# Optimization experiments

Hardware: AMD Instinct MI355X
Metric: run time of the kernel (lower is better)

## Reference

```python
import jax, jax.numpy as jnp
import numpy as np

V, D, H, LYR, W, L, B = 32000, 1024, 16, 4, 256, 2048, 1
HD = D // H          # 64
I = 3280             # _round_to_multiple(3.2*D, 8)
EPS = 1e-5
STD = 0.01
CLAMP = 50.0


def rmsnorm(x, w):
    # RMSNorm with clamp/eps/isfinite guards as in the torch module
    x = jnp.clip(x.astype(jnp.float32), -10000.0, 10000.0)
    rms = jnp.sqrt(jnp.maximum(jnp.mean(x * x, axis=-1, keepdims=True), EPS) + EPS)
    out = x / rms * w
    return jnp.where(jnp.isfinite(out), out, 0.0)


def attention(x, wq_w, wq_b, wk_w, wk_b, wv_w, wv_b, wo_w, wo_b, qn_w, kn_w):
    Bx, Lx, Dx = x.shape
    def proj(w, b):
        return (x @ w.T + b).reshape(Bx, Lx, H, HD).transpose(0, 2, 1, 3)  # (B,H,L,hd)
    q = rmsnorm(proj(wq_w, wq_b), qn_w)
    k = rmsnorm(proj(wk_w, wk_b), kn_w)
    v = proj(wv_w, wv_b)
    i = jnp.arange(Lx)
    # causal + sliding-window: mask out j > i  OR  i - j >= window
    invalid = (i[None, :] > i[:, None]) | ((i[:, None] - i[None, :]) >= W)
    scores = jnp.einsum('bhqd,bhkd->bhqk', q, k) * (HD ** -0.5)
    scores = jnp.where(invalid[None, None], -jnp.inf, scores)
    probs = jax.nn.softmax(scores, axis=-1)
    out = jnp.einsum('bhqk,bhkd->bhqd', probs, v)
    out = jnp.where(jnp.isfinite(out), out, 0.0)
    out = out.transpose(0, 2, 1, 3).reshape(Bx, Lx, Dx)
    return out @ wo_w.T + wo_b


def swiglu(x, w1_w, w1_b, w2_w, w2_b, w3_w, w3_b):
    z1 = x @ w1_w.T + w1_b
    z3 = x @ w3_w.T + w3_b
    return (jax.nn.silu(z1) * z3) @ w2_w.T + w2_b


def setup_inputs() -> dict:
    key = jax.random.key(0)
    ks = jax.random.split(key, 12)
    nrm = lambda k, s: jax.random.normal(k, s, jnp.float32) * STD
    return {
        'tokens': jax.random.randint(ks[0], (B, L), 0, V, dtype=jnp.int32),
        'embed_w': nrm(ks[1], (V, D)),
        'ln1_w': jnp.ones((LYR, D), jnp.float32),
        'ln2_w': jnp.ones((LYR, D), jnp.float32),
        'wq_w': nrm(ks[2], (LYR, D, D)), 'wq_b': jnp.zeros((LYR, D), jnp.float32),
        'wk_w': nrm(ks[3], (LYR, D, D)), 'wk_b': jnp.zeros((LYR, D), jnp.float32),
        'wv_w': nrm(ks[4], (LYR, D, D)), 'wv_b': jnp.zeros((LYR, D), jnp.float32),
        'wo_w': nrm(ks[5], (LYR, D, D)), 'wo_b': jnp.zeros((LYR, D), jnp.float32),
        'qn_w': jnp.ones((LYR, HD), jnp.float32),
        'kn_w': jnp.ones((LYR, HD), jnp.float32),
        'w1_w': nrm(ks[6], (LYR, I, D)), 'w1_b': jnp.zeros((LYR, I), jnp.float32),
        'w2_w': nrm(ks[7], (LYR, D, I)), 'w2_b': jnp.zeros((LYR, D), jnp.float32),
        'w3_w': nrm(ks[8], (LYR, I, D)), 'w3_b': jnp.zeros((LYR, I), jnp.float32),
        'lnf_w': jnp.ones((D,), jnp.float32),
        'lm_w': nrm(ks[9], (V, D)), 'lm_b': jnp.zeros((V,), jnp.float32),
    }


def reference(tokens, embed_w, ln1_w, ln2_w, wq_w, wq_b, wk_w, wk_b, wv_w, wv_b,
              wo_w, wo_b, qn_w, kn_w, w1_w, w1_b, w2_w, w2_b, w3_w, w3_b,
              lnf_w, lm_w, lm_b):
    x = embed_w[tokens]  # (B,L,D)
    for l in range(LYR):
        x = x + attention(rmsnorm(x, ln1_w[l]),
                          wq_w[l], wq_b[l], wk_w[l], wk_b[l], wv_w[l], wv_b[l],
                          wo_w[l], wo_b[l], qn_w[l], kn_w[l])
        x = x + swiglu(rmsnorm(x, ln2_w[l]),
                       w1_w[l], w1_b[l], w2_w[l], w2_b[l], w3_w[l], w3_b[l])
    x = rmsnorm(x, lnf_w)
    logits = x @ lm_w.T + lm_b
    return jnp.clip(logits, -CLAMP, CLAMP)
```

## Files before the change

### kernel.cpp

```cpp
#include <hip/hip_runtime.h>
#include <hip/hip_bf16.h>
#include <math.h>

#define Dm   1024
#define Hn   16
#define HDm  64
#define Lm   2048
#define Wm   256
#define Im   3280
#define Vm   32000
#define NLAYER 4
#define EPSf 1e-5f

typedef unsigned short ushort;
typedef __attribute__((ext_vector_type(8))) short bf16x8;
typedef __attribute__((ext_vector_type(4))) float f32x4;

static __device__ __forceinline__ float clamp10k(float x) {
    return fminf(fmaxf(x, -10000.0f), 10000.0f);
}

static __device__ __forceinline__ ushort f2bf(float f) {
    __hip_bfloat16 h = __float2bfloat16(f);
    return *reinterpret_cast<ushort*>(&h);
}

static __device__ __forceinline__ void gload16(const ushort* g, ushort* l) {
    __builtin_amdgcn_global_load_lds(
        (const __attribute__((address_space(1))) void*)(const void*)g,
        (__attribute__((address_space(3))) void*)(void*)l, 16, 0, 0);
}

__global__ __launch_bounds__(256) void embed_k(const int* __restrict__ tok,
                                               const float* __restrict__ ew,
                                               float* __restrict__ x) {
    int i = blockIdx.x;
    int t = tok[i];
    const float4* src = (const float4*)(ew + (size_t)t * Dm);
    float4* dst = (float4*)(x + (size_t)i * Dm);
    dst[threadIdx.x] = src[threadIdx.x];
}

__global__ __launch_bounds__(256) void rmsnorm_row(const float* __restrict__ x,
                                                   const float* __restrict__ w,
                                                   ushort* __restrict__ out) {
    __shared__ float red[256];
    int row = blockIdx.x, tid = threadIdx.x;
    float4 vx = ((const float4*)(x + (size_t)row * Dm))[tid];
    vx.x = clamp10k(vx.x); vx.y = clamp10k(vx.y);
    vx.z = clamp10k(vx.z); vx.w = clamp10k(vx.w);
    float ss = vx.x * vx.x + vx.y * vx.y + vx.z * vx.z + vx.w * vx.w;
    red[tid] = ss;
    __syncthreads();
    for (int s = 128; s > 0; s >>= 1) {
        if (tid < s) red[tid] += red[tid + s];
        __syncthreads();
    }
    float mean = red[0] * (1.0f / Dm);
    float inv = 1.0f / sqrtf(fmaxf(mean, EPSf) + EPSf);
    float4 vw = ((const float4*)w)[tid];
    float o0 = vx.x * inv * vw.x;
    float o1 = vx.y * inv * vw.y;
    float o2 = vx.z * inv * vw.z;
    float o3 = vx.w * inv * vw.w;
    if (!isfinite(o0)) o0 = 0.0f;
    if (!isfinite(o1)) o1 = 0.0f;
    if (!isfinite(o2)) o2 = 0.0f;
    if (!isfinite(o3)) o3 = 0.0f;
    ushort4 o;
    o.x = f2bf(o0); o.y = f2bf(o1); o.z = f2bf(o2); o.w = f2bf(o3);
    ((ushort4*)(out + (size_t)row * Dm))[tid] = o;
}

__global__ __launch_bounds__(256) void rmsnorm_head_bf16(const float* __restrict__ qk,
                                                         const float* __restrict__ w,
                                                         ushort* __restrict__ out) {
    int wave = threadIdx.x >> 6, lane = threadIdx.x & 63;
    int r = blockIdx.x * 4 + wave;
    int i = r >> 4, h = r & 15;
    float xv = clamp10k(qk[(size_t)r * HDm + lane]);
    float ss = xv * xv;
#pragma unroll
    for (int off = 32; off >= 1; off >>= 1) ss += __shfl_xor(ss, off, 64);
    float mean = ss * (1.0f / HDm);
    float inv = 1.0f / sqrtf(fmaxf(mean, EPSf) + EPSf);
    float o = xv * inv * w[lane];
    if (!isfinite(o)) o = 0.0f;
    out[((size_t)h * Lm + i) * HDm + lane] = f2bf(o);
}

__global__ __launch_bounds__(256) void vtrans_k(const float* __restrict__ vb,
                                                ushort* __restrict__ vt) {
    __shared__ ushort tile[64 * 72];
    int i0 = blockIdx.x * 64, h = blockIdx.y;
    int t = threadIdx.x;
    int r = t >> 2, q4 = t & 3;
    const float4* src = (const float4*)(vb + (size_t)(i0 + r) * Dm + h * HDm);
#pragma unroll
    for (int k = 0; k < 4; ++k) {
        int c4 = q4 + k * 4;
        float4 v = src[c4];
        int c = c4 * 4;
        tile[(c + 0) * 72 + r] = f2bf(v.x);
        tile[(c + 1) * 72 + r] = f2bf(v.y);
        tile[(c + 2) * 72 + r] = f2bf(v.z);
        tile[(c + 3) * 72 + r] = f2bf(v.w);
    }
    __syncthreads();
    int d = t >> 2, ch = t & 3;
    uint4 a = *(const uint4*)&tile[d * 72 + ch * 16];
    uint4 b = *(const uint4*)&tile[d * 72 + ch * 16 + 8];
    ushort* dst = vt + ((size_t)(h * HDm + d)) * Lm + i0 + ch * 16;
    *(uint4*)dst = a;
    *(uint4*)(dst + 8) = b;
}

__global__ __launch_bounds__(256) void attn_mfma(const ushort* __restrict__ qh,
                                                 const ushort* __restrict__ kh,
                                                 const ushort* __restrict__ vt,
                                                 ushort* __restrict__ out) {
    __shared__ ushort Ks[32 * 72];
    __shared__ ushort Vs[64 * 40];
    __shared__ ushort Pl[4][16 * 40];

    const int tid  = threadIdx.x;
    const int wave = tid >> 6;
    const int lane = tid & 63;
    const int l15  = lane & 15;
    const int quad = lane >> 4;
    const int h    = blockIdx.y;
    const int q0   = blockIdx.x * 64;
    const int qw   = q0 + wave * 16;
    const int qmy  = qw + l15;

    const ushort* qbase = qh + ((size_t)h * Lm + qw + l15) * HDm;
    bf16x8 qf0 = *(const bf16x8*)(qbase + quad * 8);
    bf16x8 qf1 = *(const bf16x8*)(qbase + 32 + quad * 8);

    f32x4 o0 = {0.f, 0.f, 0.f, 0.f}, o1 = o0, o2 = o0, o3 = o0;
    float m = -1e4f, lsum = 0.0f;

    const int krow = tid >> 3, kch = tid & 7;
    const int vrow = tid >> 2, vch = tid & 3;
    const ushort* kg = kh + ((size_t)h * Lm + krow) * HDm + kch * 8;
    const ushort* vg = vt + ((size_t)(h * HDm + vrow)) * Lm + vch * 8;

    int tlo = q0 - 256; if (tlo < 0) tlo = 0;

    for (int t0 = tlo; t0 < q0 + 64; t0 += 32) {
        __syncthreads();
        *(uint4*)&Ks[krow * 72 + kch * 8] = *(const uint4*)(kg + (size_t)t0 * HDm);
        *(uint4*)&Vs[vrow * 40 + vch * 8] = *(const uint4*)(vg + t0);
        __syncthreads();

        if (t0 <= qw + 15 && t0 + 31 >= qw - 255) {
            bf16x8 k00 = *(const bf16x8*)&Ks[l15 * 72 + quad * 8];
            bf16x8 k01 = *(const bf16x8*)&Ks[l15 * 72 + 32 + quad * 8];
            bf16x8 k10 = *(const bf16x8*)&Ks[(l15 + 16) * 72 + quad * 8];
            bf16x8 k11 = *(const bf16x8*)&Ks[(l15 + 16) * 72 + 32 + quad * 8];
            f32x4 s0 = {0.f, 0.f, 0.f, 0.f}, s1 = s0;
            s0 = __builtin_amdgcn_mfma_f32_16x16x32_bf16(k00, qf0, s0, 0, 0, 0);
            s0 = __builtin_amdgcn_mfma_f32_16x16x32_bf16(k01, qf1, s0, 0, 0, 0);
            s1 = __builtin_amdgcn_mfma_f32_16x16x32_bf16(k10, qf0, s1, 0, 0, 0);
            s1 = __builtin_amdgcn_mfma_f32_16x16x32_bf16(k11, qf1, s1, 0, 0, 0);

            float sv[8];
            bool full = (t0 + 31 <= qw) && (t0 >= qw - 240);
            int jb = t0 + quad * 4;
            if (full) {
#pragma unroll
                for (int r = 0; r < 4; ++r) {
                    sv[r]     = s0[r] * 0.125f;
                    sv[r + 4] = s1[r] * 0.125f;
                }
            } else {
#pragma unroll
                for (int r = 0; r < 4; ++r) {
                    int ja = jb + r, jc = jb + 16 + r;
                    sv[r]     = (ja <= qmy && ja >= qmy - 255) ? s0[r] * 0.125f : -1e30f;
                    sv[r + 4] = (jc <= qmy && jc >= qmy - 255) ? s1[r] * 0.125f : -1e30f;
                }
            }

            float rm = sv[0];
#pragma unroll
            for (int r = 1; r < 8; ++r) rm = fmaxf(rm, sv[r]);
            rm = fmaxf(rm, __shfl_xor(rm, 16));
            rm = fmaxf(rm, __shfl_xor(rm, 32));
            float mn = fmaxf(m, rm);
            float alpha = __expf(m - mn);
            float p[8], ps = 0.f;
#pragma unroll
            for (int r = 0; r < 8; ++r) { p[r] = __expf(sv[r] - mn); ps += p[r]; }
            ps += __shfl_xor(ps, 16);
            ps += __shfl_xor(ps, 32);
            lsum = lsum * alpha + ps;
            m = mn;

            ushort4 pk0, pk1;
            pk0.x = f2bf(p[0]); pk0.y = f2bf(p[1]); pk0.z = f2bf(p[2]); pk0.w = f2bf(p[3]);
            pk1.x = f2bf(p[4]); pk1.y = f2bf(p[5]); pk1.z = f2bf(p[6]); pk1.w = f2bf(p[7]);
            *(ushort4*)&Pl[wave][l15 * 40 + quad * 4]      = pk0;
            *(ushort4*)&Pl[wave][l15 * 40 + 16 + quad * 4] = pk1;
            asm volatile("s_waitcnt lgkmcnt(0)" ::: "memory");
            bf16x8 pa  = *(const bf16x8*)&Pl[wave][l15 * 40 + quad * 8];
            bf16x8 vf0 = *(const bf16x8*)&Vs[l15 * 40 + quad * 8];
            bf16x8 vf1 = *(const bf16x8*)&Vs[(l15 + 16) * 40 + quad * 8];
            bf16x8 vf2 = *(const bf16x8*)&Vs[(l15 + 32) * 40 + quad * 8];
            bf16x8 vf3 = *(const bf16x8*)&Vs[(l15 + 48) * 40 + quad * 8];

            float a0 = __shfl(alpha, quad * 4 + 0);
            float a1 = __shfl(alpha, quad * 4 + 1);
            float a2 = __shfl(alpha, quad * 4 + 2);
            float a3 = __shfl(alpha, quad * 4 + 3);
            o0[0] *= a0; o0[1] *= a1; o0[2] *= a2; o0[3] *= a3;
            o1[0] *= a0; o1[1] *= a1; o1[2] *= a2; o1[3] *= a3;
            o2[0] *= a0; o2[1] *= a1; o2[2] *= a2; o2[3] *= a3;
            o3[0] *= a0; o3[1] *= a1; o3[2] *= a2; o3[3] *= a3;

            o0 = __builtin_amdgcn_mfma_f32_16x16x32_bf16(pa, vf0, o0, 0, 0, 0);
            o1 = __builtin_amdgcn_mfma_f32_16x16x32_bf16(pa, vf1, o1, 0, 0, 0);
            o2 = __builtin_amdgcn_mfma_f32_16x16x32_bf16(pa, vf2, o2, 0, 0, 0);
            o3 = __builtin_amdgcn_mfma_f32_16x16x32_bf16(pa, vf3, o3, 0, 0, 0);
        }
    }

    float linv = 1.0f / lsum;
    ushort* ob = out + (size_t)(qw + quad * 4) * Dm + h * HDm + l15;
#pragma unroll
    for (int r = 0; r < 4; ++r) {
        float li = __shfl(linv, quad * 4 + r);
        size_t off = (size_t)r * Dm;
        ob[off]      = f2bf(o0[r] * li);
        ob[off + 16] = f2bf(o1[r] * li);
        ob[off + 32] = f2bf(o2[r] * li);
        ob[off + 48] = f2bf(o3[r] * li);
    }
}

__global__ __launch_bounds__(256) void convert_w(const float* __restrict__ src,
                                                 ushort* __restrict__ dst,
                                                 int N, int K, int Kp) {
    int n = blockIdx.y;
    int k = blockIdx.x * 256 + threadIdx.x;
    if (k >= Kp) return;
    float v = 0.0f;
    if (n < N && k < K) v = src[(size_t)n * K + k];
    dst[(size_t)n * Kp + k] = f2bf(v);
}

__global__ __launch_bounds__(256) void gemm_bf16(const ushort* __restrict__ A,
                                                 const ushort* __restrict__ Wb,
                                                 const float* __restrict__ bias,
                                                 float* __restrict__ C,
                                                 int K, int N, int ldc, int act) {
    __shared__ ushort As[128 * 32];
    __shared__ ushort Bs[128 * 32];
    const int tid = threadIdx.x;
    const int wave = tid >> 6;
    const int lane = tid & 63;
    const int lane15 = lane & 15;
    const int quad = lane >> 4;
    const int rowBlk = blockIdx.y * 128;
    const int colBlk = blockIdx.x * 128;
    const int wm = (wave >> 1) * 64;
    const int wn = (wave & 1) * 64;

    const int srow = lane >> 2;
    const int scol = (lane & 3) * 8;

    const ushort* aSrc0 = A + (size_t)(rowBlk + wave * 32 + srow) * K + scol;
    const ushort* bSrc0 = Wb + (size_t)(colBlk + wave * 32 + srow) * K + scol;
    ushort* aDst0 = &As[(wave * 32) * 32];
    ushort* aDst1 = &As[(wave * 32 + 16) * 32];
    ushort* bDst0 = &Bs[(wave * 32) * 32];
    ushort* bDst1 = &Bs[(wave * 32 + 16) * 32];

    f32x4 acc[4][4];
#pragma unroll
    for (int i = 0; i < 4; ++i)
#pragma unroll
        for (int j = 0; j < 4; ++j) acc[i][j] = (f32x4){0.f, 0.f, 0.f, 0.f};

    for (int k0 = 0; k0 < K; k0 += 32) {
        __syncthreads();
        gload16(aSrc0 + k0, aDst0);
        gload16(aSrc0 + k0 + (size_t)16 * K, aDst1);
        gload16(bSrc0 + k0, bDst0);
        gload16(bSrc0 + k0 + (size_t)16 * K, bDst1);
        __syncthreads();

        bf16x8 a[4], b[4];
#pragma unroll
        for (int im = 0; im < 4; ++im)
            a[im] = *(const bf16x8*)&As[(wm + im * 16 + lane15) * 32 + quad * 8];
#pragma unroll
        for (int in = 0; in < 4; ++in)
            b[in] = *(const bf16x8*)&Bs[(wn + in * 16 + lane15) * 32 + quad * 8];
#pragma unroll
        for (int im = 0; im < 4; ++im)
#pragma unroll
            for (int in = 0; in < 4; ++in)
                acc[im][in] = __builtin_amdgcn_mfma_f32_16x16x32_bf16(
                    a[im], b[in], acc[im][in], 0, 0, 0);
    }

#pragma unroll
    for (int im = 0; im < 4; ++im) {
        int r0 = rowBlk + wm + im * 16 + quad * 4;
#pragma unroll
        for (int in = 0; in < 4; ++in) {
            int c = colBlk + wn + in * 16 + lane15;
            if (c < N) {
                float bia = bias[c];
#pragma unroll
                for (int reg = 0; reg < 4; ++reg) {
                    float v = acc[im][in][reg] + bia;
                    if (act) v = fminf(fmaxf(v, -50.0f), 50.0f);
                    C[(size_t)(r0 + reg) * ldc + c] = v;
                }
            }
        }
    }
}

__global__ __launch_bounds__(256) void add_k(float* __restrict__ x,
                                             const float* __restrict__ t, int n4) {
    int i = blockIdx.x * 256 + threadIdx.x;
    if (i < n4) {
        float4 a = ((const float4*)x)[i];
        float4 b = ((const float4*)t)[i];
        a.x += b.x; a.y += b.y; a.z += b.z; a.w += b.w;
        ((float4*)x)[i] = a;
    }
}

__global__ __launch_bounds__(256) void swiglu_k(const float* __restrict__ z1,
                                                const float* __restrict__ z3,
                                                ushort* __restrict__ z1b) {
    int row = blockIdx.x, tid = threadIdx.x;
    const float* a = z1 + (size_t)row * Im;
    const float* b = z3 + (size_t)row * Im;
    ushort* o = z1b + (size_t)row * 3296;
    for (int c = tid; c < 3296; c += 256) {
        float v = 0.0f;
        if (c < Im) {
            float x = a[c];
            v = x / (1.0f + expf(-x)) * b[c];
        }
        o[c] = f2bf(v);
    }
}

extern "C" void kernel_launch(void* const* d_in, const int* in_sizes, int n_in,
                              void* d_out, int out_size, void* d_ws, size_t ws_size,
                              hipStream_t stream) {
    const int*   tokens  = (const int*)  d_in[0];
    const float* embed_w = (const float*)d_in[1];
    const float* ln1_w   = (const float*)d_in[2];
    const float* ln2_w   = (const float*)d_in[3];
    const float* wq_w    = (const float*)d_in[4];
    const float* wq_b    = (const float*)d_in[5];
    const float* wk_w    = (const float*)d_in[6];
    const float* wk_b    = (const float*)d_in[7];
    const float* wv_w    = (const float*)d_in[8];
    const float* wv_b    = (const float*)d_in[9];
    const float* wo_w    = (const float*)d_in[10];
    const float* wo_b    = (const float*)d_in[11];
    const float* qn_w    = (const float*)d_in[12];
    const float* kn_w    = (const float*)d_in[13];
    const float* w1_w    = (const float*)d_in[14];
    const float* w1_b    = (const float*)d_in[15];
    const float* w2_w    = (const float*)d_in[16];
    const float* w2_b    = (const float*)d_in[17];
    const float* w3_w    = (const float*)d_in[18];
    const float* w3_b    = (const float*)d_in[19];
    const float* lnf_w   = (const float*)d_in[20];
    const float* lm_w    = (const float*)d_in[21];
    const float* lm_b    = (const float*)d_in[22];
    float* out = (float*)d_out;

    const size_t MB = 1ull << 20;
    char* base = (char*)d_ws;
    float*  x    = (float*)(base);
    ushort* xn   = (ushort*)(base + 8 * MB);
    float*  t2   = (float*)(base + 12 * MB);
    float*  qb   = (float*)(base + 20 * MB);
    float*  kb   = (float*)(base + 28 * MB);
    float*  vb   = (float*)(base + 36 * MB);
    ushort* attb = (ushort*)(base + 44 * MB);
    ushort* qhb  = (ushort*)(base + 48 * MB);
    ushort* khb  = (ushort*)(base + 52 * MB);
    ushort* vtb  = (ushort*)(base + 56 * MB);
    float*  z1   = (float*)(base + 20 * MB);
    float*  z3   = (float*)(base + 48 * MB);
    ushort* z1b  = (ushort*)(base + 75 * MB);
    ushort* wbuf = (ushort*)(base + 89 * MB);

    const size_t LD = (size_t)Lm * Dm;
    int nLD4 = (int)(LD / 4);

    dim3 gemmD(8, 16);
    dim3 gemmI(26, 16);
    dim3 gemmC(63, 16);

    embed_k<<<Lm, 256, 0, stream>>>(tokens, embed_w, x);

    for (int l = 0; l < NLAYER; ++l) {
        size_t oDD = (size_t)l * Dm * Dm, oD = (size_t)l * Dm;
        size_t oID = (size_t)l * Im * Dm, oI = (size_t)l * Im;
        size_t oH = (size_t)l * HDm;

        rmsnorm_row<<<Lm, 256, 0, stream>>>(x, ln1_w + oD, xn);

        convert_w<<<dim3(4, 1024), 256, 0, stream>>>(wq_w + oDD, wbuf, Dm, Dm, Dm);
        gemm_bf16<<<gemmD, 256, 0, stream>>>(xn, wbuf, wq_b + oD, qb, Dm, Dm, Dm, 0);
        convert_w<<<dim3(4, 1024), 256, 0, stream>>>(wk_w + oDD, wbuf, Dm, Dm, Dm);
        gemm_bf16<<<gemmD, 256, 0, stream>>>(xn, wbuf, wk_b + oD, kb, Dm, Dm, Dm, 0);
        convert_w<<<dim3(4, 1024), 256, 0, stream>>>(wv_w + oDD, wbuf, Dm, Dm, Dm);
        gemm_bf16<<<gemmD, 256, 0, stream>>>(xn, wbuf, wv_b + oD, vb, Dm, Dm, Dm, 0);

        rmsnorm_head_bf16<<<(Lm * Hn) / 4, 256, 0, stream>>>(qb, qn_w + oH, qhb);
        rmsnorm_head_bf16<<<(Lm * Hn) / 4, 256, 0, stream>>>(kb, kn_w + oH, khb);
        vtrans_k<<<dim3(Lm / 64, Hn), 256, 0, stream>>>(vb, vtb);
        attn_mfma<<<dim3(Lm / 64, Hn), 256, 0, stream>>>(qhb, khb, vtb, attb);

        convert_w<<<dim3(4, 1024), 256, 0, stream>>>(wo_w + oDD, wbuf, Dm, Dm, Dm);
        gemm_bf16<<<gemmD, 256, 0, stream>>>(attb, wbuf, wo_b + oD, t2, Dm, Dm, Dm, 0);
        add_k<<<(nLD4 + 255) / 256, 256, 0, stream>>>(x, t2, nLD4);

        rmsnorm_row<<<Lm, 256, 0, stream>>>(x, ln2_w + oD, xn);

        convert_w<<<dim3(4, 3328), 256, 0, stream>>>(w1_w + oID, wbuf, Im, Dm, Dm);
        gemm_bf16<<<gemmI, 256, 0, stream>>>(xn, wbuf, w1_b + oI, z1, Dm, Im, Im, 0);
        convert_w<<<dim3(4, 3328), 256, 0, stream>>>(w3_w + oID, wbuf, Im, Dm, Dm);
        gemm_bf16<<<gemmI, 256, 0, stream>>>(xn, wbuf, w3_b + oI, z3, Dm, Im, Im, 0);
        swiglu_k<<<Lm, 256, 0, stream>>>(z1, z3, z1b);

        convert_w<<<dim3(13, 1024), 256, 0, stream>>>(w2_w + oID, wbuf, Dm, Im, 3296);
        gemm_bf16<<<gemmD, 256, 0, stream>>>(z1b, wbuf, w2_b + oD, t2, 3296, Dm, Dm, 0);
        add_k<<<(nLD4 + 255) / 256, 256, 0, stream>>>(x, t2, nLD4);
    }

    rmsnorm_row<<<Lm, 256, 0, stream>>>(x, lnf_w, xn);
    for (int c = 0; c < 4; ++c) {
        convert_w<<<dim3(4, 8064), 256, 0, stream>>>(lm_w + (size_t)c * 8000 * Dm,
                                                     wbuf, 8000, Dm, Dm);
        gemm_bf16<<<gemmC, 256, 0, stream>>>(xn, wbuf, lm_b + c * 8000,
                                             out + c * 8000, Dm, 8000, Vm, 1);
    }
}
```

Before: 2.255 ms.

## Fuse QKV and W1/W3 GEMMs, fold residual add into GEMM, widen K tile

Concatenates the Q/K/V weights into one N=3072 GEMM and the W1/W3 weights into one N=6656 GEMM, so the activation tile is reused and fewer launches run. The residual add is folded into the GEMM epilogue through a new res pointer, which removes the separate add kernels and their round trip through memory. The GEMM K-step is doubled to 64 with a larger LDS tile, halving the barriers per K. Risks are higher LDS use, which may lower occupancy, and in-place aliasing where res and C are the same buffer; that is safe here because each element is read and then written by the same thread.

Measured after the change: 2.071 ms. -8.1%, faster.

```diff
diff --git a/kernel.cpp b/kernel.cpp
--- a/kernel.cpp
+++ b/kernel.cpp
@@ -11,6 +11,10 @@
 #define Vm   32000
 #define NLAYER 4
 #define EPSf 1e-5f
+#define QKVN 3072
+#define FFN  6560
+#define FFNP 6656
+#define IP   3328
 
 typedef unsigned short ushort;
 typedef __attribute__((ext_vector_type(8))) short bf16x8;
@@ -78,7 +82,7 @@
     int wave = threadIdx.x >> 6, lane = threadIdx.x & 63;
     int r = blockIdx.x * 4 + wave;
     int i = r >> 4, h = r & 15;
-    float xv = clamp10k(qk[(size_t)r * HDm + lane]);
+    float xv = clamp10k(qk[(size_t)i * QKVN + h * HDm + lane]);
     float ss = xv * xv;
 #pragma unroll
     for (int off = 32; off >= 1; off >>= 1) ss += __shfl_xor(ss, off, 64);
@@ -95,7 +99,7 @@
     int i0 = blockIdx.x * 64, h = blockIdx.y;
     int t = threadIdx.x;
     int r = t >> 2, q4 = t & 3;
-    const float4* src = (const float4*)(vb + (size_t)(i0 + r) * Dm + h * HDm);
+    const float4* src = (const float4*)(vb + (size_t)(i0 + r) * QKVN + h * HDm);
 #pragma unroll
     for (int k = 0; k < 4; ++k) {
         int c4 = q4 + k * 4;
@@ -249,13 +253,28 @@
     dst[(size_t)n * Kp + k] = f2bf(v);
 }
 
+__global__ __launch_bounds__(256) void cat3_k(float* __restrict__ dst,
+                                              const float* __restrict__ a, int na,
+                                              const float* __restrict__ b, int nb,
+                                              const float* __restrict__ c, int nc,
+                                              int ntot) {
+    int i = blockIdx.x * 256 + threadIdx.x;
+    if (i >= ntot) return;
+    float v = 0.0f;
+    if (i < na) v = a[i];
+    else if (i < na + nb) v = b[i - na];
+    else if (i < na + nb + nc) v = c[i - na - nb];
+    dst[i] = v;
+}
+
 __global__ __launch_bounds__(256) void gemm_bf16(const ushort* __restrict__ A,
                                                  const ushort* __restrict__ Wb,
                                                  const float* __restrict__ bias,
+                                                 const float* __restrict__ res,
                                                  float* __restrict__ C,
                                                  int K, int N, int ldc, int act) {
-    __shared__ ushort As[128 * 32];
-    __shared__ ushort Bs[128 * 32];
+    __shared__ ushort As[128 * 64];
+    __shared__ ushort Bs[128 * 64];
     const int tid = threadIdx.x;
     const int wave = tid >> 6;
     const int lane = tid & 63;
@@ -266,15 +285,13 @@
     const int wm = (wave >> 1) * 64;
     const int wn = (wave & 1) * 64;
 
-    const int srow = lane >> 2;
-    const int scol = (lane & 3) * 8;
-
-    const ushort* aSrc0 = A + (size_t)(rowBlk + wave * 32 + srow) * K + scol;
-    const ushort* bSrc0 = Wb + (size_t)(colBlk + wave * 32 + srow) * K + scol;
-    ushort* aDst0 = &As[(wave * 32) * 32];
-    ushort* aDst1 = &As[(wave * 32 + 16) * 32];
-    ushort* bDst0 = &Bs[(wave * 32) * 32];
-    ushort* bDst1 = &Bs[(wave * 32 + 16) * 32];
+    const int srow = lane >> 3;
+    const int scol = (lane & 7) * 8;
+
+    const ushort* aSrc = A + (size_t)(rowBlk + wave * 32 + srow) * K + scol;
+    const ushort* bSrc = Wb + (size_t)(colBlk + wave * 32 + srow) * K + scol;
+    ushort* aD = &As[(wave * 32) * 64];
+    ushort* bD = &Bs[(wave * 32) * 64];
 
     f32x4 acc[4][4];
 #pragma unroll
@@ -282,27 +299,31 @@
 #pragma unroll
         for (int j = 0; j < 4; ++j) acc[i][j] = (f32x4){0.f, 0.f, 0.f, 0.f};
 
-    for (int k0 = 0; k0 < K; k0 += 32) {
+    for (int k0 = 0; k0 < K; k0 += 64) {
         __syncthreads();
-        gload16(aSrc0 + k0, aDst0);
-        gload16(aSrc0 + k0 + (size_t)16 * K, aDst1);
-        gload16(bSrc0 + k0, bDst0);
-        gload16(bSrc0 + k0 + (size_t)16 * K, bDst1);
+#pragma unroll
+        for (int g = 0; g < 4; ++g) {
+            gload16(aSrc + k0 + (size_t)(g * 8) * K, aD + g * 8 * 64);
+            gload16(bSrc + k0 + (size_t)(g * 8) * K, bD + g * 8 * 64);
+        }
         __syncthreads();
 
-        bf16x8 a[4], b[4];
-#pragma unroll
-        for (int im = 0; im < 4; ++im)
-            a[im] = *(const bf16x8*)&As[(wm + im * 16 + lane15) * 32 + quad * 8];
-#pragma unroll
-        for (int in = 0; in < 4; ++in)
-            b[in] = *(const bf16x8*)&Bs[(wn + in * 16 + lane15) * 32 + quad * 8];
-#pragma unroll
-        for (int im = 0; im < 4; ++im)
+#pragma unroll
+        for (int kk = 0; kk < 2; ++kk) {
+            bf16x8 a[4], b[4];
+#pragma unroll
+            for (int im = 0; im < 4; ++im)
+                a[im] = *(const bf16x8*)&As[(wm + im * 16 + lane15) * 64 + kk * 32 + quad * 8];
 #pragma unroll
             for (int in = 0; in < 4; ++in)
-                acc[im][in] = __builtin_amdgcn_mfma_f32_16x16x32_bf16(
-                    a[im], b[in], acc[im][in], 0, 0, 0);
+                b[in] = *(const bf16x8*)&Bs[(wn + in * 16 + lane15) * 64 + kk * 32 + quad * 8];
+#pragma unroll
+            for (int im = 0; im < 4; ++im)
+#pragma unroll
+                for (int in = 0; in < 4; ++in)
+                    acc[im][in] = __builtin_amdgcn_mfma_f32_16x16x32_bf16(
+                        a[im], b[in], acc[im][in], 0, 0, 0);
+        }
     }
 
 #pragma unroll
@@ -317,36 +338,25 @@
                 for (int reg = 0; reg < 4; ++reg) {
                     float v = acc[im][in][reg] + bia;
                     if (act) v = fminf(fmaxf(v, -50.0f), 50.0f);
-                    C[(size_t)(r0 + reg) * ldc + c] = v;
+                    size_t idx = (size_t)(r0 + reg) * ldc + c;
+                    if (res) v += res[idx];
+                    C[idx] = v;
                 }
             }
         }
     }
 }
 
-__global__ __launch_bounds__(256) void add_k(float* __restrict__ x,
-                                             const float* __restrict__ t, int n4) {
-    int i = blockIdx.x * 256 + threadIdx.x;
-    if (i < n4) {
-        float4 a = ((const float4*)x)[i];
-        float4 b = ((const float4*)t)[i];
-        a.x += b.x; a.y += b.y; a.z += b.z; a.w += b.w;
-        ((float4*)x)[i] = a;
-    }
-}
-
-__global__ __launch_bounds__(256) void swiglu_k(const float* __restrict__ z1,
-                                                const float* __restrict__ z3,
+__global__ __launch_bounds__(256) void swiglu_k(const float* __restrict__ z13,
                                                 ushort* __restrict__ z1b) {
     int row = blockIdx.x, tid = threadIdx.x;
-    const float* a = z1 + (size_t)row * Im;
-    const float* b = z3 + (size_t)row * Im;
-    ushort* o = z1b + (size_t)row * 3296;
-    for (int c = tid; c < 3296; c += 256) {
+    const float* r = z13 + (size_t)row * FFNP;
+    ushort* o = z1b + (size_t)row * IP;
+    for (int c = tid; c < IP; c += 256) {
         float v = 0.0f;
         if (c < Im) {
-            float x = a[c];
-            v = x / (1.0f + expf(-x)) * b[c];
+            float x = r[c];
+            v = x / (1.0f + expf(-x)) * r[Im + c];
         }
         o[c] = f2bf(v);
     }
@@ -384,24 +394,20 @@
     char* base = (char*)d_ws;
     float*  x    = (float*)(base);
     ushort* xn   = (ushort*)(base + 8 * MB);
-    float*  t2   = (float*)(base + 12 * MB);
-    float*  qb   = (float*)(base + 20 * MB);
-    float*  kb   = (float*)(base + 28 * MB);
-    float*  vb   = (float*)(base + 36 * MB);
-    ushort* attb = (ushort*)(base + 44 * MB);
-    ushort* qhb  = (ushort*)(base + 48 * MB);
-    ushort* khb  = (ushort*)(base + 52 * MB);
-    ushort* vtb  = (ushort*)(base + 56 * MB);
-    float*  z1   = (float*)(base + 20 * MB);
-    float*  z3   = (float*)(base + 48 * MB);
-    ushort* z1b  = (ushort*)(base + 75 * MB);
-    ushort* wbuf = (ushort*)(base + 89 * MB);
-
-    const size_t LD = (size_t)Lm * Dm;
-    int nLD4 = (int)(LD / 4);
-
-    dim3 gemmD(8, 16);
-    dim3 gemmI(26, 16);
+    float*  qkvb = (float*)(base + 16 * MB);
+    ushort* attb = (ushort*)(base + 42 * MB);
+    ushort* qhb  = (ushort*)(base + 46 * MB);
+    ushort* khb  = (ushort*)(base + 50 * MB);
+    ushort* vtb  = (ushort*)(base + 54 * MB);
+    float*  z13  = (float*)(base + 16 * MB);
+    ushort* z1b  = (ushort*)(base + 72 * MB);
+    ushort* wbuf = (ushort*)(base + 88 * MB);
+    float*  bqkv = (float*)(base + 106 * MB);
+    float*  b13  = (float*)(base + 107 * MB);
+
+    dim3 gemmQKV(24, 16);
+    dim3 gemmO(8, 16);
+    dim3 gemm13(52, 16);
     dim3 gemmC(63, 16);
 
     embed_k<<<Lm, 256, 0, stream>>>(tokens, embed_w, x);
@@ -413,40 +419,48 @@
 
         rmsnorm_row<<<Lm, 256, 0, stream>>>(x, ln1_w + oD, xn);
 
+        cat3_k<<<12, 256, 0, stream>>>(bqkv, wq_b + oD, Dm, wk_b + oD, Dm,
+                                       wv_b + oD, Dm, QKVN);
         convert_w<<<dim3(4, 1024), 256, 0, stream>>>(wq_w + oDD, wbuf, Dm, Dm, Dm);
-        gemm_bf16<<<gemmD, 256, 0, stream>>>(xn, wbuf, wq_b + oD, qb, Dm, Dm, Dm, 0);
-        convert_w<<<dim3(4, 1024), 256, 0, stream>>>(wk_w + oDD, wbuf, Dm, Dm, Dm);
-        gemm_bf16<<<gemmD, 256, 0, stream>>>(xn, wbuf, wk_b + oD, kb, Dm, Dm, Dm, 0);
-        convert_w<<<dim3(4, 1024), 256, 0, stream>>>(wv_w + oDD, wbuf, Dm, Dm, Dm);
-        gemm_bf16<<<gemmD, 256, 0, stream>>>(xn, wbuf, wv_b + oD, vb, Dm, Dm, Dm, 0);
-
-        rmsnorm_head_bf16<<<(Lm * Hn) / 4, 256, 0, stream>>>(qb, qn_w + oH, qhb);
-        rmsnorm_head_bf16<<<(Lm * Hn) / 4, 256, 0, stream>>>(kb, kn_w + oH, khb);
-        vtrans_k<<<dim3(Lm / 64, Hn), 256, 0, stream>>>(vb, vtb);
+        convert_w<<<dim3(4, 1024), 256, 0, stream>>>(wk_w + oDD,
+                                                     wbuf + (size_t)Dm * Dm, Dm, Dm, Dm);
+        convert_w<<<dim3(4, 1024), 256, 0, stream>>>(wv_w + oDD,
+                                                     wbuf + (size_t)2 * Dm * Dm, Dm, Dm, Dm);
+        gemm_bf16<<<gemmQKV, 256, 0, stream>>>(xn, wbuf, bqkv, nullptr, qkvb,
+                                               Dm, QKVN, QKVN, 0);
+
+        rmsnorm_head_bf16<<<(Lm * Hn) / 4, 256, 0, stream>>>(qkvb, qn_w + oH, qhb);
+        rmsnorm_head_bf16<<<(Lm * Hn) / 4, 256, 0, stream>>>(qkvb + Dm, kn_w + oH, khb);
+        vtrans_k<<<dim3(Lm / 64, Hn), 256, 0, stream>>>(qkvb + 2 * Dm, vtb);
         attn_mfma<<<dim3(Lm / 64, Hn), 256, 0, stream>>>(qhb, khb, vtb, attb);
 
         convert_w<<<dim3(4, 1024), 256, 0, stream>>>(wo_w + oDD, wbuf, Dm, Dm, Dm);
-        gemm_bf16<<<gemmD, 256, 0, stream>>>(attb, wbuf, wo_b + oD, t2, Dm, Dm, Dm, 0);
-        add_k<<<(nLD4 + 255) / 256, 256, 0, stream>>>(x, t2, nLD4);
+        gemm_bf16<<<gemmO, 256, 0, stream>>>(attb, wbuf, wo_b + oD, x, x,
+                                             Dm, Dm, Dm, 0);
 
         rmsnorm_row<<<Lm, 256, 0, stream>>>(x, ln2_w + oD, xn);
 
-        convert_w<<<dim3(4, 3328), 256, 0, stream>>>(w1_w + oID, wbuf, Im, Dm, Dm);
-        gemm_bf16<<<gemmI, 256, 0, stream>>>(xn, wbuf, w1_b + oI, z1, Dm, Im, Im, 0);
-        convert_w<<<dim3(4, 3328), 256, 0, stream>>>(w3_w + oID, wbuf, Im, Dm, Dm);
-        gemm_bf16<<<gemmI, 256, 0, stream>>>(xn, wbuf, w3_b + oI, z3, Dm, Im, Im, 0);
-        swiglu_k<<<Lm, 256, 0, stream>>>(z1, z3, z1b);
-
-        convert_w<<<dim3(13, 1024), 256, 0, stream>>>(w2_w + oID, wbuf, Dm, Im, 3296);
-        gemm_bf16<<<gemmD, 256, 0, stream>>>(z1b, wbuf, w2_b + oD, t2, 3296, Dm, Dm, 0);
-        add_k<<<(nLD4 + 255) / 256, 256, 0, stream>>>(x, t2, nLD4);
+        cat3_k<<<26, 256, 0, stream>>>(b13, w1_b + oI, Im, w3_b + oI, Im,
+                                       w1_b + oI, 0, FFNP);
+        convert_w<<<dim3(4, 3280), 256, 0, stream>>>(w1_w + oID, wbuf, Im, Dm, Dm);
+        convert_w<<<dim3(4, 3280), 256, 0, stream>>>(w3_w + oID,
+                                                     wbuf + (size_t)Im * Dm, Im, Dm, Dm);
+        convert_w<<<dim3(4, 96), 256, 0, stream>>>(w1_w + oID,
+                                                   wbuf + (size_t)FFN * Dm, 0, Dm, Dm);
+        gemm_bf16<<<gemm13, 256, 0, stream>>>(xn, wbuf, b13, nullptr, z13,
+                                              Dm, FFN, FFNP, 0);
+        swiglu_k<<<Lm, 256, 0, stream>>>(z13, z1b);
+
+        convert_w<<<dim3(13, 1024), 256, 0, stream>>>(w2_w + oID, wbuf, Dm, Im, IP);
+        gemm_bf16<<<gemmO, 256, 0, stream>>>(z1b, wbuf, w2_b + oD, x, x,
+                                             IP, Dm, Dm, 0);
     }
 
     rmsnorm_row<<<Lm, 256, 0, stream>>>(x, lnf_w, xn);
     for (int c = 0; c < 4; ++c) {
         convert_w<<<dim3(4, 8064), 256, 0, stream>>>(lm_w + (size_t)c * 8000 * Dm,
                                                      wbuf, 8000, Dm, Dm);
-        gemm_bf16<<<gemmC, 256, 0, stream>>>(xn, wbuf, lm_b + c * 8000,
+        gemm_bf16<<<gemmC, 256, 0, stream>>>(xn, wbuf, lm_b + c * 8000, nullptr,
                                              out + c * 8000, Dm, 8000, Vm, 1);
     }
 }
```
